# Kernel tuning notes

Hardware: AMD Instinct MI355X
Metric: run time of the kernel (lower is better)

## Reference

```python
import jax, jax.numpy as jnp
import numpy as np


def setup_inputs() -> dict:
    key = jax.random.key(0)
    kx, ka = jax.random.split(key)
    B, N, D = 8, 4096, 32
    x = jax.random.normal(kx, (B, N, D), dtype=jnp.float32)
    # adjacency-like nonnegative weights (dense branch of GsumLayer)
    a = jax.random.uniform(ka, (B, N, N), dtype=jnp.float32)
    return {"x": x, "a": a}


def reference(x, a):
    # GsumLayer dense branch: out[b] = a[b] @ x[b]  -> [B, N, D]
    return jnp.einsum('bnm,bmd->bnd', a, x)
```

## Files before the change

kernel.cpp:

```cpp
#include <hip/hip_runtime.h>


#define GN 4096
#define GD 32
#define ROWS 64
#define BK 64
#define APAD 4

__global__ __launch_bounds__(256, 2) void gsum_kernel(
    const float* __restrict__ x,
    const float* __restrict__ a,
    float* __restrict__ out)
{
    __shared__ float As[ROWS][BK + APAD];
    __shared__ float Xs[BK][GD];

    const int t    = threadIdx.x;
    const int b    = blockIdx.x >> 6;
    const int tile = blockIdx.x & 63;
    const long long row0 = (long long)tile * ROWS;

    const float* Ab = a   + ((long long)b * GN + row0) * GN;
    const float* Xb = x   + (long long)b * GN * GD;
    float*       Ob = out + ((long long)b * GN + row0) * GD;

    const int g = t & 7;
    const int r = t >> 3;

    const int sr = t >> 2;
    const int sc = (t & 3) * 4;

    float4 acc0 = {0.f, 0.f, 0.f, 0.f};
    float4 acc1 = {0.f, 0.f, 0.f, 0.f};

    for (int k0 = 0; k0 < GN; k0 += BK) {
        __syncthreads();

        {
            const float* Arow = Ab + (long long)sr * GN + k0;
            #pragma unroll
            for (int i = 0; i < 4; ++i) {
                float4 v = *(const float4*)(Arow + sc + i * 16);
                *(float4*)&As[sr][sc + i * 16] = v;
            }
        }
        {
            const float* Xrow = Xb + (long long)(k0 + sr) * GD;
            float4 v0 = *(const float4*)(Xrow + sc);
            float4 v1 = *(const float4*)(Xrow + 16 + sc);
            *(float4*)&Xs[sr][sc]      = v0;
            *(float4*)&Xs[sr][16 + sc] = v1;
        }

        __syncthreads();

        #pragma unroll
        for (int kk = 0; kk < BK; kk += 4) {
            float4 a0 = *(const float4*)&As[r][kk];
            float4 a1 = *(const float4*)&As[r + 32][kk];
            #pragma unroll
            for (int j = 0; j < 4; ++j) {
                float4 xv = *(const float4*)&Xs[kk + j][g * 4];
                float aj0 = (j == 0) ? a0.x : (j == 1) ? a0.y : (j == 2) ? a0.z : a0.w;
                float aj1 = (j == 0) ? a1.x : (j == 1) ? a1.y : (j == 2) ? a1.z : a1.w;
                acc0.x += aj0 * xv.x; acc0.y += aj0 * xv.y;
                acc0.z += aj0 * xv.z; acc0.w += aj0 * xv.w;
                acc1.x += aj1 * xv.x; acc1.y += aj1 * xv.y;
                acc1.z += aj1 * xv.z; acc1.w += aj1 * xv.w;
            }
        }
    }

    *(float4*)(Ob + (long long)r        * GD + g * 4) = acc0;
    *(float4*)(Ob + (long long)(r + 32) * GD + g * 4) = acc1;
}

extern "C" void kernel_launch(void* const* d_in, const int* in_sizes, int n_in,
                              void* d_out, int out_size, void* d_ws, size_t ws_size,
                              hipStream_t stream) {
    const float* x = (const float*)d_in[0];
    const float* a = (const float*)d_in[1];
    float* out = (float*)d_out;

    const int B = 8;
    const int tiles_per_batch = GN / ROWS;
    dim3 grid(B * tiles_per_batch);
    dim3 block(256);
    gsum_kernel<<<grid, block, 0, stream>>>(x, a, out);
}
```

Baseline: 743.7 us.

## Split-K over M with register-blocked A loads and separate reduction kernel

```diff
diff --git a/kernel.cpp b/kernel.cpp
--- a/kernel.cpp
+++ b/kernel.cpp
@@ -1,78 +1,86 @@
 #include <hip/hip_runtime.h>
 
 
-#define GN 4096
-#define GD 32
-#define ROWS 64
-#define BK 64
-#define APAD 4
+#define N_ 4096
+#define D_ 32
+#define MSPLIT 16
+#define MCHUNK (N_ / MSPLIT)
+#define PART_ELEMS (8 * N_ * D_)
 
-__global__ __launch_bounds__(256, 2) void gsum_kernel(
+__global__ __launch_bounds__(256, 4) void gsum_stage1(
     const float* __restrict__ x,
     const float* __restrict__ a,
-    float* __restrict__ out)
+    float* __restrict__ part)
 {
-    __shared__ float As[ROWS][BK + APAD];
-    __shared__ float Xs[BK][GD];
+    __shared__ float Xs[MCHUNK * D_];
 
-    const int t    = threadIdx.x;
-    const int b    = blockIdx.x >> 6;
-    const int tile = blockIdx.x & 63;
-    const long long row0 = (long long)tile * ROWS;
+    const int t  = threadIdx.x;
+    const int rb = blockIdx.x;
+    const int ms = blockIdx.y;
+    const int b  = rb >> 4;
+    const int n0 = (rb & 15) * 256;
+    const int m0 = ms * MCHUNK;
 
-    const float* Ab = a   + ((long long)b * GN + row0) * GN;
-    const float* Xb = x   + (long long)b * GN * GD;
-    float*       Ob = out + ((long long)b * GN + row0) * GD;
+    {
+        const float4* src = (const float4*)(x + ((long long)b * N_ + m0) * D_);
+        float4* dst = (float4*)Xs;
+        #pragma unroll
+        for (int j = 0; j < 8; ++j)
+            dst[t + j * 256] = src[t + j * 256];
+    }
+    __syncthreads();
 
-    const int g = t & 7;
-    const int r = t >> 3;
+    const int g   = t & 7;
+    const int r   = (t >> 3) & 7;
+    const int wid = t >> 6;
+    const int row_base = n0 + wid * 64 + r * 8;
 
-    const int sr = t >> 2;
-    const int sc = (t & 3) * 4;
+    const float* ap = a + ((long long)(b * N_ + row_base)) * N_ + m0;
 
-    float4 acc0 = {0.f, 0.f, 0.f, 0.f};
-    float4 acc1 = {0.f, 0.f, 0.f, 0.f};
+    float4 acc[8];
+    #pragma unroll
+    for (int i = 0; i < 8; ++i) acc[i] = make_float4(0.f, 0.f, 0.f, 0.f);
 
-    for (int k0 = 0; k0 < GN; k0 += BK) {
-        __syncthreads();
-
-        {
-            const float* Arow = Ab + (long long)sr * GN + k0;
+    for (int mm = 0; mm < MCHUNK; mm += 4) {
+        float4 av[8];
+        #pragma unroll
+        for (int i = 0; i < 8; ++i)
+            av[i] = *(const float4*)(ap + (long long)i * N_ + mm);
+        #pragma unroll
+        for (int j = 0; j < 4; ++j) {
+            float4 xv = *(const float4*)&Xs[(mm + j) * D_ + g * 4];
             #pragma unroll
-            for (int i = 0; i < 4; ++i) {
-                float4 v = *(const float4*)(Arow + sc + i * 16);
-                *(float4*)&As[sr][sc + i * 16] = v;
-            }
-        }
-        {
-            const float* Xrow = Xb + (long long)(k0 + sr) * GD;
-            float4 v0 = *(const float4*)(Xrow + sc);
-            float4 v1 = *(const float4*)(Xrow + 16 + sc);
-            *(float4*)&Xs[sr][sc]      = v0;
-            *(float4*)&Xs[sr][16 + sc] = v1;
-        }
-
-        __syncthreads();
-
-        #pragma unroll
-        for (int kk = 0; kk < BK; kk += 4) {
-            float4 a0 = *(const float4*)&As[r][kk];
-            float4 a1 = *(const float4*)&As[r + 32][kk];
-            #pragma unroll
-            for (int j = 0; j < 4; ++j) {
-                float4 xv = *(const float4*)&Xs[kk + j][g * 4];
-                float aj0 = (j == 0) ? a0.x : (j == 1) ? a0.y : (j == 2) ? a0.z : a0.w;
-                float aj1 = (j == 0) ? a1.x : (j == 1) ? a1.y : (j == 2) ? a1.z : a1.w;
-                acc0.x += aj0 * xv.x; acc0.y += aj0 * xv.y;
-                acc0.z += aj0 * xv.z; acc0.w += aj0 * xv.w;
-                acc1.x += aj1 * xv.x; acc1.y += aj1 * xv.y;
-                acc1.z += aj1 * xv.z; acc1.w += aj1 * xv.w;
+            for (int i = 0; i < 8; ++i) {
+                float aj = (j == 0) ? av[i].x : (j == 1) ? av[i].y
+                         : (j == 2) ? av[i].z : av[i].w;
+                acc[i].x += aj * xv.x;
+                acc[i].y += aj * xv.y;
+                acc[i].z += aj * xv.z;
+                acc[i].w += aj * xv.w;
             }
         }
     }
 
-    *(float4*)(Ob + (long long)r        * GD + g * 4) = acc0;
-    *(float4*)(Ob + (long long)(r + 32) * GD + g * 4) = acc1;
+    float* op = part + (long long)ms * PART_ELEMS
+                     + ((long long)(b * N_ + row_base)) * D_ + g * 4;
+    #pragma unroll
+    for (int i = 0; i < 8; ++i)
+        *(float4*)(op + i * D_) = acc[i];
+}
+
+__global__ __launch_bounds__(256, 4) void gsum_reduce(
+    const float* __restrict__ part,
+    float* __restrict__ out)
+{
+    const int idx = blockIdx.x * 256 + threadIdx.x;
+    const float4* p = (const float4*)part;
+    float4 s = p[idx];
+    #pragma unroll
+    for (int sft = 1; sft < MSPLIT; ++sft) {
+        float4 v = p[idx + (long long)sft * (PART_ELEMS / 4)];
+        s.x += v.x; s.y += v.y; s.z += v.z; s.w += v.w;
+    }
+    ((float4*)out)[idx] = s;
 }
 
 extern "C" void kernel_launch(void* const* d_in, const int* in_sizes, int n_in,
@@ -80,11 +88,12 @@
                               hipStream_t stream) {
     const float* x = (const float*)d_in[0];
     const float* a = (const float*)d_in[1];
-    float* out = (float*)d_out;
+    float* out  = (float*)d_out;
+    float* part = (float*)d_ws;
 
-    const int B = 8;
-    const int tiles_per_batch = GN / ROWS;
-    dim3 grid(B * tiles_per_batch);
-    dim3 block(256);
-    gsum_kernel<<<grid, block, 0, stream>>>(x, a, out);
+    dim3 grid1(128, MSPLIT);
+    gsum_stage1<<<grid1, 256, 0, stream>>>(x, a, part);
+
+    dim3 grid2(PART_ELEMS * MSPLIT / 4 / 256 / MSPLIT);
+    gsum_reduce<<<grid2, 256, 0, stream>>>(part, out);
 }
```

Result: slower. 885.5 us (+19.1%).
